# Kernel tuning notes

Measured on AMD Instinct MI355X. Metric: run time of the kernel, lower is better.

The kernel has to match this reference:

```python
import jax, jax.numpy as jnp
import numpy as np

H, B, F, D1, D21, D22, C = 10, 16384, 4, 2048, 2048, 2048, 2
OBS_X, OBS_Y, RADIUS = 40.0, 15.0, 6.0


def setup_inputs() -> dict:
    key = jax.random.key(0)
    ks = jax.random.split(key, 12)
    s = 0.02  # weight scale
    return {
        'x':   jax.random.normal(ks[0], (B, F), jnp.float32),
        'W1':  jax.random.normal(ks[1], (H, F, D1), jnp.float32) * s,
        'b1':  jnp.zeros((H, D1), jnp.float32),
        'W21': jax.random.normal(ks[2], (H, D1, D21), jnp.float32) * s,
        'b21': jnp.zeros((H, D21), jnp.float32),
        'W22': jax.random.normal(ks[3], (H, D1, D22), jnp.float32) * s,
        'b22': jnp.zeros((H, D22), jnp.float32),
        'W31': jax.random.normal(ks[4], (H, D21, C), jnp.float32) * s,
        'b31': jnp.zeros((H, C), jnp.float32),
        'W32': jax.random.normal(ks[5], (H, D22, C), jnp.float32) * s,
        'b32': jnp.zeros((H, C), jnp.float32),
        'wt':  jnp.ones((H,), jnp.float32),
        'mean': jax.random.normal(ks[6], (F,), jnp.float32),
        'std':  jnp.ones((F,), jnp.float32),
        'sgn': 1,
        'itr': 0,
    }


def reference(x, W1, b1, W21, b21, W22, b22, W31, b31, W32, b32, wt, mean, std, sgn, itr):
    # x: [B,F]; un-normalized state x0 = x*std + mean
    x0 = x * std + mean

    # --- 10-head small-MLP ensemble (batched over heads via einsum) ---
    h1  = jax.nn.relu(jnp.einsum('bf,hfd->hbd', x, W1) + b1[:, None, :])      # [H,B,D1]
    x21 = jax.nn.relu(jnp.einsum('hbd,hde->hbe', h1, W21) + b21[:, None, :])  # [H,B,D21]
    x22 = jax.nn.relu(jnp.einsum('hbd,hde->hbe', h1, W22) + b22[:, None, :])  # [H,B,D22]
    x31 = jnp.einsum('hbe,hec->hbc', x21, W31) + b31[:, None, :]              # [H,B,C] nominal control
    x32 = 4.0 * jax.nn.sigmoid(jnp.einsum('hbe,hec->hbc', x22, W32) + b32[:, None, :])  # [H,B,C] CBF params

    # --- dCBF constraint (shared across heads; depends only on x0) ---
    px, py, theta, v = x0[:, 0], x0[:, 1], x0[:, 2], x0[:, 3]
    dx, dy = px - OBS_X, py - OBS_Y
    st, ct = jnp.sin(theta), jnp.cos(theta)
    barrier = dx * dx + dy * dy - RADIUS * RADIUS                 # [B]
    barrier_dot = 2.0 * dx * v * ct + 2.0 * dy * v * st          # [B]
    Lf2b = 2.0 * v * v                                            # [B]
    LgLfbu1 = -2.0 * dx * v * st + 2.0 * dy * v * ct
    LgLfbu2 = 2.0 * dx * ct + 2.0 * dy * st
    G = jnp.stack([-LgLfbu1, -LgLfbu2], axis=-1)                  # [B,C]

    # sgn == 1 -> same branch for every head (i==0 or sgn==1)
    h_rhs = Lf2b + (x32[..., 0] + x32[..., 1]) * barrier_dot + x32[..., 0] * x32[..., 1] * barrier  # [H,B]

    # --- batched QP: min 0.5 u'u - x31'u  s.t. G u <= h  (Q = I) ---
    # closed-form single-constraint active set: u = x31 - relu(G.x31 - h)/||G||^2 * G
    Gu = jnp.einsum('bc,hbc->hb', G, x31)                         # [H,B]
    GG = jnp.sum(G * G, axis=-1)                                  # [B]
    lam = jax.nn.relu(Gu - h_rhs) / GG                            # [H,B]
    u = x31 - lam[..., None] * G[None, :, :]                      # [H,B,C]

    # --- softmax-weighted ensemble sum ---
    w = jax.nn.softmax(wt)                                        # [H]
    return jnp.einsum('h,hbc->bc', w, u)                          # [B,C]
```

## Files before the change

### kernel.cpp

```cpp
#include <hip/hip_runtime.h>
#include <hip/hip_bf16.h>
#include <stdint.h>

#define H_  10
#define B_  16384
#define F_  4
#define D_  2048
#define C_  2

typedef __attribute__((ext_vector_type(8))) short  short8;
typedef __attribute__((ext_vector_type(4))) float  floatx4;
typedef __attribute__((ext_vector_type(2))) float  float2v;

typedef const uint32_t __attribute__((address_space(1))) gu32;
typedef uint32_t       __attribute__((address_space(3))) lu32;

__device__ __forceinline__ void async16(const void* g, void* l) {
    __builtin_amdgcn_global_load_lds((gu32*)g, (lu32*)l, 16, 0, 0);
}

__device__ __forceinline__ uint32_t packbf(float a, float b) {
    a = fmaxf(a, 0.f); b = fmaxf(b, 0.f);
    const uint32_t ax = __builtin_bit_cast(uint32_t, a) + 0x8000u;
    const uint32_t bx = __builtin_bit_cast(uint32_t, b) + 0x8000u;
    return (ax >> 16) | (bx & 0xFFFF0000u);
}

__device__ __forceinline__ uint32_t f2bf(float f) {
    union { float f; uint32_t u; } a; a.f = f;
    uint32_t u = a.u;
    u += 0x7FFF + ((u >> 16) & 1);
    return u >> 16;
}
__device__ __forceinline__ uint32_t pack2bf(float a, float b) {
    return f2bf(a) | (f2bf(b) << 16);
}


__global__ __launch_bounds__(256) void k_convert(
    const float* __restrict__ W21, const float* __restrict__ W22,
    uint16_t* __restrict__ W21t, uint16_t* __restrict__ W22t)
{
    __shared__ float tile[64][65];
    const int z = blockIdx.z;
    const int h = z % H_;
    const float* src = (z < H_ ? W21 : W22) + (size_t)h * D_ * D_;
    uint16_t*   dst  = (z < H_ ? W21t : W22t) + (size_t)h * D_ * D_;
    const int k0 = blockIdx.x * 64, n0 = blockIdx.y * 64;
    const int t = threadIdx.x;

    const int c4 = (t & 15) * 4;
    const int rb = (t >> 4) * 4;
#pragma unroll
    for (int i = 0; i < 4; i++) {
        const float4 v = *(const float4*)(src + (size_t)(k0 + rb + i) * D_ + n0 + c4);
        tile[rb + i][c4 + 0] = v.x; tile[rb + i][c4 + 1] = v.y;
        tile[rb + i][c4 + 2] = v.z; tile[rb + i][c4 + 3] = v.w;
    }
    __syncthreads();
    const int n = t >> 2;
    const int cb = (t & 3) * 2;
#pragma unroll
    for (int j = 0; j < 2; j++) {
        const int kk = (cb + j) * 8;
        uint32_t pk[4];
#pragma unroll
        for (int e = 0; e < 4; e++)
            pk[e] = pack2bf(tile[kk + 2 * e][n], tile[kk + 2 * e + 1][n]);
        *(uint4*)(dst + (size_t)(n0 + n) * D_ + k0 + kk) = make_uint4(pk[0], pk[1], pk[2], pk[3]);
    }
}

__global__ __launch_bounds__(256) void k_zero(uint4* p, int n4) {
    const int i = blockIdx.x * 256 + threadIdx.x;
    if (i < n4) p[i] = make_uint4(0u, 0u, 0u, 0u);
}

__global__ __launch_bounds__(256, 2) void k_gemm(
    const float* __restrict__ x, const float* __restrict__ W1, const float* __restrict__ b1,
    const uint16_t* __restrict__ W21t, const uint16_t* __restrict__ W22t,
    const float* __restrict__ b21, const float* __restrict__ b22,
    const float* __restrict__ W31, const float* __restrict__ W32,
    float* __restrict__ acc31, float* __restrict__ acc32)
{
    __shared__ uint4 At[1024];
    __shared__ uint4 Bt0[1024];
    __shared__ uint4 Bt1[1024];

    const int h = blockIdx.z;
    const int mBase = blockIdx.x * 128;
    const int nBase = blockIdx.y * 128;
    const int t = threadIdx.x;
    const int lane = t & 63, wid = t >> 6;
    const int q = lane >> 4, c15 = lane & 15;
    const int wm = wid >> 1, wn = wid & 1;

    const int k0 = (t & 7) * 8;
    const int mg = (t >> 3) * 4;

    float xv[4][4];
#pragma unroll
    for (int i = 0; i < 4; i++) {
        const float4 v = *(const float4*)(x + (size_t)(mBase + mg + i) * F_);
        xv[i][0] = v.x; xv[i][1] = v.y; xv[i][2] = v.z; xv[i][3] = v.w;
    }

    const int nb = wid * 32 + (lane >> 3);
    const int chunk = (lane & 7) ^ ((lane >> 3) & 7);
    const uint16_t* bsrc0 = W21t + (size_t)h * D_ * D_ + (size_t)(nBase + nb) * D_ + chunk * 8;
    const uint16_t* bsrc1 = W22t + (size_t)h * D_ * D_ + (size_t)(nBase + nb) * D_ + chunk * 8;

    const float* W1h = W1 + (size_t)h * F_ * D_;
    const float* b1h = b1 + (size_t)h * D_;

    floatx4 acc0[4][4], acc1[4][4];
    const floatx4 z4 = {0.f, 0.f, 0.f, 0.f};
#pragma unroll
    for (int mi = 0; mi < 4; mi++)
#pragma unroll
        for (int ni = 0; ni < 4; ni++) { acc0[mi][ni] = z4; acc1[mi][ni] = z4; }

    for (int kt = 0; kt < D_; kt += 64) {
        float2v w1v[4][4], b1v[4];
        {
            const float4 bb0 = *(const float4*)(b1h + kt + k0);
            const float4 bb1 = *(const float4*)(b1h + kt + k0 + 4);
            b1v[0] = (float2v){bb0.x, bb0.y}; b1v[1] = (float2v){bb0.z, bb0.w};
            b1v[2] = (float2v){bb1.x, bb1.y}; b1v[3] = (float2v){bb1.z, bb1.w};
#pragma unroll
            for (int f = 0; f < 4; f++) {
                const float4 a0 = *(const float4*)(W1h + f * D_ + kt + k0);
                const float4 a1 = *(const float4*)(W1h + f * D_ + kt + k0 + 4);
                w1v[f][0] = (float2v){a0.x, a0.y}; w1v[f][1] = (float2v){a0.z, a0.w};
                w1v[f][2] = (float2v){a1.x, a1.y}; w1v[f][3] = (float2v){a1.z, a1.w};
            }
        }
#pragma unroll
        for (int i = 0; i < 4; i++) {
            async16(bsrc0 + kt + i * (8 * D_), (char*)Bt0 + wid * 4096 + i * 1024);
            async16(bsrc1 + kt + i * (8 * D_), (char*)Bt1 + wid * 4096 + i * 1024);
        }
#pragma unroll
        for (int i = 0; i < 4; i++) {
            const int m = mg + i;
            float2v hv[4];
#pragma unroll
            for (int j = 0; j < 4; j++) hv[j] = b1v[j];
#pragma unroll
            for (int f = 0; f < 4; f++) {
                const float2v xs = {xv[i][f], xv[i][f]};
#pragma unroll
                for (int j = 0; j < 4; j++)
                    hv[j] = __builtin_elementwise_fma(xs, w1v[f][j], hv[j]);
            }
            At[m * 8 + ((t & 7) ^ (m & 7))] =
                make_uint4(packbf(hv[0].x, hv[0].y), packbf(hv[1].x, hv[1].y),
                           packbf(hv[2].x, hv[2].y), packbf(hv[3].x, hv[3].y));
        }
        __syncthreads();
#pragma unroll
        for (int s = 0; s < 2; s++) {
            short8 af[4];
#pragma unroll
            for (int mi = 0; mi < 4; mi++) {
                const int m = wm * 64 + mi * 16 + c15;
                af[mi] = __builtin_bit_cast(short8, At[m * 8 + ((s * 4 + q) ^ (c15 & 7))]);
            }
#pragma unroll
            for (int ni = 0; ni < 4; ni++) {
                const int n = wn * 64 + ni * 16 + c15;
                const int bidx = n * 8 + ((s * 4 + q) ^ (c15 & 7));
                const short8 bf0 = __builtin_bit_cast(short8, Bt0[bidx]);
#pragma unroll
                for (int mi = 0; mi < 4; mi++)
                    acc0[mi][ni] = __builtin_amdgcn_mfma_f32_16x16x32_bf16(af[mi], bf0, acc0[mi][ni], 0, 0, 0);
                const short8 bf1 = __builtin_bit_cast(short8, Bt1[bidx]);
#pragma unroll
                for (int mi = 0; mi < 4; mi++)
                    acc1[mi][ni] = __builtin_amdgcn_mfma_f32_16x16x32_bf16(af[mi], bf1, acc1[mi][ni], 0, 0, 0);
            }
        }
        __syncthreads();
    }

#pragma unroll
    for (int p = 0; p < 2; p++) {
        const float* b2p = (p == 0 ? b21 : b22) + (size_t)h * D_;
        const float* W3p = (p == 0 ? W31 : W32) + (size_t)h * D_ * C_;
        float* ab = (p == 0 ? acc31 : acc32) + (size_t)h * B_ * C_;
        float w3x[4], w3y[4], bs[4];
#pragma unroll
        for (int ni = 0; ni < 4; ni++) {
            const int n = nBase + wn * 64 + ni * 16 + c15;
            bs[ni] = b2p[n];
            const float2 w2 = *(const float2*)(W3p + n * 2);
            w3x[ni] = w2.x; w3y[ni] = w2.y;
        }
        float s0[16], s1[16];
#pragma unroll
        for (int mi = 0; mi < 4; mi++)
#pragma unroll
            for (int r = 0; r < 4; r++) {
                float t0 = 0.f, t1 = 0.f;
#pragma unroll
                for (int ni = 0; ni < 4; ni++) {
                    float v = (p == 0 ? acc0[mi][ni][r] : acc1[mi][ni][r]) + bs[ni];
                    v = fmaxf(v, 0.f);
                    t0 = fmaf(v, w3x[ni], t0);
                    t1 = fmaf(v, w3y[ni], t1);
                }
                s0[mi * 4 + r] = t0; s1[mi * 4 + r] = t1;
            }
#pragma unroll
        for (int off = 1; off < 16; off <<= 1)
#pragma unroll
            for (int i = 0; i < 16; i++) {
                s0[i] += __shfl_xor(s0[i], off, 64);
                s1[i] += __shfl_xor(s1[i], off, 64);
            }
        if (c15 == 0) {
#pragma unroll
            for (int mi = 0; mi < 4; mi++)
#pragma unroll
                for (int r = 0; r < 4; r++) {
                    const int row = mBase + wm * 64 + mi * 16 + q * 4 + r;
                    atomicAdd(&ab[row * C_ + 0], s0[mi * 4 + r]);
                    atomicAdd(&ab[row * C_ + 1], s1[mi * 4 + r]);
                }
        }
    }
}

__global__ __launch_bounds__(256) void k_final(
    const float* __restrict__ x,
    const float* __restrict__ acc31, const float* __restrict__ acc32,
    const float* __restrict__ b31, const float* __restrict__ b32,
    const float* __restrict__ wt, const float* __restrict__ mean,
    const float* __restrict__ stdv, float* __restrict__ out)
{
    const int b = blockIdx.x * 256 + threadIdx.x;
    const float4 xb = *(const float4*)(x + (size_t)b * 4);
    const float px = xb.x * stdv[0] + mean[0];
    const float py = xb.y * stdv[1] + mean[1];
    const float th = xb.z * stdv[2] + mean[2];
    const float v  = xb.w * stdv[3] + mean[3];
    const float dx = px - 40.0f, dy = py - 15.0f;
    const float st = sinf(th), ct = cosf(th);
    const float barrier = dx * dx + dy * dy - 36.0f;
    const float bdot = 2.f * dx * v * ct + 2.f * dy * v * st;
    const float Lf2b = 2.f * v * v;
    const float G0 = -(-2.f * dx * v * st + 2.f * dy * v * ct);
    const float G1 = -(2.f * dx * ct + 2.f * dy * st);
    const float GG = G0 * G0 + G1 * G1;

    float we[H_];
    float wmax = wt[0];
    for (int h = 1; h < H_; h++) wmax = fmaxf(wmax, wt[h]);
    float wsum = 0.f;
    for (int h = 0; h < H_; h++) { we[h] = expf(wt[h] - wmax); wsum += we[h]; }

    float o0 = 0.f, o1 = 0.f;
#pragma unroll
    for (int h = 0; h < H_; h++) {
        const size_t idx = ((size_t)h * B_ + b) * 2;
        const float x310 = acc31[idx]     + b31[h * 2];
        const float x311 = acc31[idx + 1] + b31[h * 2 + 1];
        const float z0 = acc32[idx]     + b32[h * 2];
        const float z1 = acc32[idx + 1] + b32[h * 2 + 1];
        const float x320 = 4.f / (1.f + expf(-z0));
        const float x321 = 4.f / (1.f + expf(-z1));
        const float hr = Lf2b + (x320 + x321) * bdot + x320 * x321 * barrier;
        const float Gu = G0 * x310 + G1 * x311;
        const float lam = fmaxf(Gu - hr, 0.f) / GG;
        o0 += we[h] * (x310 - lam * G0);
        o1 += we[h] * (x311 - lam * G1);
    }
    out[b * 2]     = o0 / wsum;
    out[b * 2 + 1] = o1 / wsum;
}

extern "C" void kernel_launch(void* const* d_in, const int* in_sizes, int n_in,
                              void* d_out, int out_size, void* d_ws, size_t ws_size,
                              hipStream_t stream)
{
    const float* x    = (const float*)d_in[0];
    const float* W1   = (const float*)d_in[1];
    const float* b1   = (const float*)d_in[2];
    const float* W21  = (const float*)d_in[3];
    const float* b21  = (const float*)d_in[4];
    const float* W22  = (const float*)d_in[5];
    const float* b22  = (const float*)d_in[6];
    const float* W31  = (const float*)d_in[7];
    const float* b31  = (const float*)d_in[8];
    const float* W32  = (const float*)d_in[9];
    const float* b32  = (const float*)d_in[10];
    const float* wt   = (const float*)d_in[11];
    const float* mean = (const float*)d_in[12];
    const float* stdv = (const float*)d_in[13];
    float* out = (float*)d_out;

    char* ws = (char*)d_ws;
    uint16_t* W21t = (uint16_t*)(ws);
    uint16_t* W22t = (uint16_t*)(ws + 83886080);
    float* acc31   = (float*)(ws + 167772160);
    float* acc32   = (float*)(ws + 169082880);

    k_convert<<<dim3(32, 32, 20), 256, 0, stream>>>(W21, W22, W21t, W22t);
    k_zero<<<dim3(640), 256, 0, stream>>>((uint4*)acc31, 163840);
    k_gemm<<<dim3(128, 16, 10), 256, 0, stream>>>(x, W1, b1, W21t, W22t,
                                                  b21, b22, W31, W32, acc31, acc32);
    k_final<<<dim3(64), 256, 0, stream>>>(x, acc31, acc32, b31, b32, wt, mean, stdv, out);
}
```

Measured before the change: 3.567 ms.

## Compute layer-1 activations in registers and double-buffer weight tiles

```diff
diff --git a/kernel.cpp b/kernel.cpp
--- a/kernel.cpp
+++ b/kernel.cpp
@@ -24,6 +24,10 @@
     const uint32_t ax = __builtin_bit_cast(uint32_t, a) + 0x8000u;
     const uint32_t bx = __builtin_bit_cast(uint32_t, b) + 0x8000u;
     return (ax >> 16) | (bx & 0xFFFF0000u);
+}
+
+__device__ __forceinline__ float2v fma2(float s, float2v a, float2v b) {
+    return __builtin_elementwise_fma((float2v){s, s}, a, b);
 }
 
 __device__ __forceinline__ uint32_t f2bf(float f) {
@@ -83,9 +87,7 @@
     const float* __restrict__ W31, const float* __restrict__ W32,
     float* __restrict__ acc31, float* __restrict__ acc32)
 {
-    __shared__ uint4 At[1024];
-    __shared__ uint4 Bt0[1024];
-    __shared__ uint4 Bt1[1024];
+    __shared__ uint4 Bt[2][2][1024];
 
     const int h = blockIdx.z;
     const int mBase = blockIdx.x * 128;
@@ -95,21 +97,18 @@
     const int q = lane >> 4, c15 = lane & 15;
     const int wm = wid >> 1, wn = wid & 1;
 
-    const int k0 = (t & 7) * 8;
-    const int mg = (t >> 3) * 4;
-
-    float xv[4][4];
-#pragma unroll
-    for (int i = 0; i < 4; i++) {
-        const float4 v = *(const float4*)(x + (size_t)(mBase + mg + i) * F_);
-        xv[i][0] = v.x; xv[i][1] = v.y; xv[i][2] = v.z; xv[i][3] = v.w;
-    }
-
     const int nb = wid * 32 + (lane >> 3);
     const int chunk = (lane & 7) ^ ((lane >> 3) & 7);
     const uint16_t* bsrc0 = W21t + (size_t)h * D_ * D_ + (size_t)(nBase + nb) * D_ + chunk * 8;
     const uint16_t* bsrc1 = W22t + (size_t)h * D_ * D_ + (size_t)(nBase + nb) * D_ + chunk * 8;
 
+    float xv[4][4];
+#pragma unroll
+    for (int mi = 0; mi < 4; mi++) {
+        const float4 v = *(const float4*)(x + (size_t)(mBase + wm * 64 + mi * 16 + c15) * F_);
+        xv[mi][0] = v.x; xv[mi][1] = v.y; xv[mi][2] = v.z; xv[mi][3] = v.w;
+    }
+
     const float* W1h = W1 + (size_t)h * F_ * D_;
     const float* b1h = b1 + (size_t)h * D_;
 
@@ -120,67 +119,77 @@
 #pragma unroll
         for (int ni = 0; ni < 4; ni++) { acc0[mi][ni] = z4; acc1[mi][ni] = z4; }
 
-    for (int kt = 0; kt < D_; kt += 64) {
-        float2v w1v[4][4], b1v[4];
-        {
-            const float4 bb0 = *(const float4*)(b1h + kt + k0);
-            const float4 bb1 = *(const float4*)(b1h + kt + k0 + 4);
-            b1v[0] = (float2v){bb0.x, bb0.y}; b1v[1] = (float2v){bb0.z, bb0.w};
-            b1v[2] = (float2v){bb1.x, bb1.y}; b1v[3] = (float2v){bb1.z, bb1.w};
-#pragma unroll
-            for (int f = 0; f < 4; f++) {
-                const float4 a0 = *(const float4*)(W1h + f * D_ + kt + k0);
-                const float4 a1 = *(const float4*)(W1h + f * D_ + kt + k0 + 4);
-                w1v[f][0] = (float2v){a0.x, a0.y}; w1v[f][1] = (float2v){a0.z, a0.w};
-                w1v[f][2] = (float2v){a1.x, a1.y}; w1v[f][3] = (float2v){a1.z, a1.w};
-            }
-        }
-#pragma unroll
-        for (int i = 0; i < 4; i++) {
-            async16(bsrc0 + kt + i * (8 * D_), (char*)Bt0 + wid * 4096 + i * 1024);
-            async16(bsrc1 + kt + i * (8 * D_), (char*)Bt1 + wid * 4096 + i * 1024);
-        }
-#pragma unroll
-        for (int i = 0; i < 4; i++) {
-            const int m = mg + i;
-            float2v hv[4];
-#pragma unroll
-            for (int j = 0; j < 4; j++) hv[j] = b1v[j];
-#pragma unroll
-            for (int f = 0; f < 4; f++) {
-                const float2v xs = {xv[i][f], xv[i][f]};
-#pragma unroll
-                for (int j = 0; j < 4; j++)
-                    hv[j] = __builtin_elementwise_fma(xs, w1v[f][j], hv[j]);
-            }
-            At[m * 8 + ((t & 7) ^ (m & 7))] =
-                make_uint4(packbf(hv[0].x, hv[0].y), packbf(hv[1].x, hv[1].y),
-                           packbf(hv[2].x, hv[2].y), packbf(hv[3].x, hv[3].y));
-        }
+#pragma unroll
+    for (int i = 0; i < 4; i++) {
+        async16(bsrc0 + i * (8 * D_), (char*)(&Bt[0][0][0]) + wid * 4096 + i * 1024);
+        async16(bsrc1 + i * (8 * D_), (char*)(&Bt[0][1][0]) + wid * 4096 + i * 1024);
+    }
+
+    for (int it = 0; it < 32; ++it) {
+        const int kt = it * 64;
+        const int cur = it & 1;
+
+        uint4 afr[2][4];
+#pragma unroll
+        for (int s = 0; s < 2; s++) {
+            const int kk = kt + s * 32 + q * 8;
+            float2v w1v[4][4], b1v[4];
+            {
+                const float4 cc0 = *(const float4*)(b1h + kk);
+                const float4 cc1 = *(const float4*)(b1h + kk + 4);
+                b1v[0] = (float2v){cc0.x, cc0.y}; b1v[1] = (float2v){cc0.z, cc0.w};
+                b1v[2] = (float2v){cc1.x, cc1.y}; b1v[3] = (float2v){cc1.z, cc1.w};
+#pragma unroll
+                for (int f = 0; f < 4; f++) {
+                    const float4 a0 = *(const float4*)(W1h + f * D_ + kk);
+                    const float4 a1 = *(const float4*)(W1h + f * D_ + kk + 4);
+                    w1v[f][0] = (float2v){a0.x, a0.y}; w1v[f][1] = (float2v){a0.z, a0.w};
+                    w1v[f][2] = (float2v){a1.x, a1.y}; w1v[f][3] = (float2v){a1.z, a1.w};
+                }
+            }
+#pragma unroll
+            for (int mi = 0; mi < 4; mi++) {
+                float2v hv[4];
+#pragma unroll
+                for (int j = 0; j < 4; j++) hv[j] = fma2(xv[mi][0], w1v[0][j], b1v[j]);
+#pragma unroll
+                for (int f = 1; f < 4; f++)
+#pragma unroll
+                    for (int j = 0; j < 4; j++) hv[j] = fma2(xv[mi][f], w1v[f][j], hv[j]);
+                afr[s][mi] = make_uint4(packbf(hv[0].x, hv[0].y), packbf(hv[1].x, hv[1].y),
+                                        packbf(hv[2].x, hv[2].y), packbf(hv[3].x, hv[3].y));
+            }
+        }
+
         __syncthreads();
+
+        if (it + 1 < 32) {
+            const int kn = kt + 64;
+#pragma unroll
+            for (int i = 0; i < 4; i++) {
+                async16(bsrc0 + kn + i * (8 * D_), (char*)(&Bt[cur ^ 1][0][0]) + wid * 4096 + i * 1024);
+                async16(bsrc1 + kn + i * (8 * D_), (char*)(&Bt[cur ^ 1][1][0]) + wid * 4096 + i * 1024);
+            }
+        }
+
 #pragma unroll
         for (int s = 0; s < 2; s++) {
-            short8 af[4];
-#pragma unroll
-            for (int mi = 0; mi < 4; mi++) {
-                const int m = wm * 64 + mi * 16 + c15;
-                af[mi] = __builtin_bit_cast(short8, At[m * 8 + ((s * 4 + q) ^ (c15 & 7))]);
-            }
 #pragma unroll
             for (int ni = 0; ni < 4; ni++) {
                 const int n = wn * 64 + ni * 16 + c15;
                 const int bidx = n * 8 + ((s * 4 + q) ^ (c15 & 7));
-                const short8 bf0 = __builtin_bit_cast(short8, Bt0[bidx]);
+                const short8 bf0 = __builtin_bit_cast(short8, Bt[cur][0][bidx]);
 #pragma unroll
                 for (int mi = 0; mi < 4; mi++)
-                    acc0[mi][ni] = __builtin_amdgcn_mfma_f32_16x16x32_bf16(af[mi], bf0, acc0[mi][ni], 0, 0, 0);
-                const short8 bf1 = __builtin_bit_cast(short8, Bt1[bidx]);
+                    acc0[mi][ni] = __builtin_amdgcn_mfma_f32_16x16x32_bf16(
+                        __builtin_bit_cast(short8, afr[s][mi]), bf0, acc0[mi][ni], 0, 0, 0);
+                const short8 bf1 = __builtin_bit_cast(short8, Bt[cur][1][bidx]);
 #pragma unroll
                 for (int mi = 0; mi < 4; mi++)
-                    acc1[mi][ni] = __builtin_amdgcn_mfma_f32_16x16x32_bf16(af[mi], bf1, acc1[mi][ni], 0, 0, 0);
-            }
-        }
-        __syncthreads();
+                    acc1[mi][ni] = __builtin_amdgcn_mfma_f32_16x16x32_bf16(
+                        __builtin_bit_cast(short8, afr[s][mi]), bf1, acc1[mi][ni], 0, 0, 0);
+            }
+        }
     }
 
 #pragma unroll
```

After: 4.165 ms. 1.17x slower.
